# Optimization experiments

Measured on AMD Instinct MI355X. Metric: run time of the kernel, lower is better.

The kernel has to match this reference:

```python
import jax, jax.numpy as jnp
import numpy as np

K = 1.0          # manifold curvature parameter (Lorentz hyperboloid <x,x>_L = -K)
NUM_HEADS = 16
LN_EPS = 1e-5
MID_EPS = 1e-8


def add_time(space):
    # lift a space-like vector onto the hyperboloid: x0 = sqrt(||s||^2 + K)
    t = jnp.sqrt(jnp.sum(space * space, axis=-1, keepdims=True) + K)
    return jnp.concatenate([t, space], axis=-1)


def hlinear(x, W, b):
    # Lorentz linear: dense map on full ambient vector -> space part, recompute time
    return add_time(jnp.einsum('...d,od->...o', x, W) + b)


def hyp_layernorm(x, g, b):
    s = x[..., 1:]
    mu = jnp.mean(s, axis=-1, keepdims=True)
    var = jnp.mean((s - mu) ** 2, axis=-1, keepdims=True)
    s = (s - mu) * jax.lax.rsqrt(var + LN_EPS) * g + b
    return add_time(s)


def hyp_relu(x):
    return add_time(jax.nn.relu(x[..., 1:]))


def lorentz_norm(v):
    # sqrt(|<v,v>_L|) with clamp for numerical safety
    inner = -v[..., 0] ** 2 + jnp.sum(v[..., 1:] ** 2, axis=-1)
    return jnp.sqrt(jnp.maximum(jnp.abs(inner), MID_EPS))


def midpoint_pair(z, x):
    # manifold.midpoint(stack([z, x], dim=-2)).squeeze(): mean then project back
    ave = 0.5 * (z + x)
    return jnp.sqrt(K) * ave / lorentz_norm(ave)[..., None]


def attention(x, Wq, bq, Wk, bk, Wv, bv, Wo, bo):
    B, S, D = x.shape
    dim = D - 1
    H = NUM_HEADS
    dh = dim // H

    def split_heads(t):
        # drop time, split space into heads, re-lift each head onto hyperboloid
        s = t[..., 1:].reshape(B, S, H, dh).transpose(0, 2, 1, 3)  # [B,H,S,dh]
        return add_time(s)                                          # [B,H,S,dh+1]

    qh = split_heads(hlinear(x, Wq, bq))
    kh = split_heads(hlinear(x, Wk, bk))
    vh = split_heads(hlinear(x, Wv, bv))

    # pairwise Lorentz inner product; scores = -d_L^2 / sqrt(dh)
    inner = (jnp.einsum('bhid,bhjd->bhij', qh[..., 1:], kh[..., 1:])
             - qh[..., 0][..., :, None] * kh[..., 0][..., None, :])
    scores = (2.0 / K + 2.0 * inner) / jnp.sqrt(jnp.asarray(dh, x.dtype))
    att = jax.nn.softmax(scores, axis=-1)

    # Lorentz midpoint aggregation of values (weights sum to 1)
    ave = jnp.einsum('bhij,bhjd->bhid', att, vh)
    out = jnp.sqrt(K) * ave / lorentz_norm(ave)[..., None]  # [B,H,S,dh+1]

    # concat head space parts, re-lift, output projection
    out_space = out[..., 1:].transpose(0, 2, 1, 3).reshape(B, S, dim)
    return hlinear(add_time(out_space), Wo, bo)


def reference(x, Wq, bq, Wk, bk, Wv, bv, Wo, bo, ln1_g, ln1_b, W1, c1, W2, c2, ln2_g, ln2_b):
    z = attention(x, Wq, bq, Wk, bk, Wv, bv, Wo, bo)
    x = midpoint_pair(z, x)
    x = hyp_layernorm(x, ln1_g, ln1_b)
    h = hyp_relu(hlinear(x, W1, c1))
    z = hlinear(h, W2, c2)
    x = midpoint_pair(z, x)
    x = hyp_layernorm(x, ln2_g, ln2_b)
    return x


def setup_inputs() -> dict:
    key = jax.random.key(0)
    ks = jax.random.split(key, 12)
    B, S, dim, mlp = 4, 1024, 1024, 4096
    D = dim + 1
    sc = 0.02
    x = add_time(jax.random.normal(ks[0], (B, S, dim), dtype=jnp.float32))
    return {
        'x': x,
        'Wq': sc * jax.random.normal(ks[1], (dim, D), dtype=jnp.float32),
        'bq': jnp.zeros((dim,), jnp.float32),
        'Wk': sc * jax.random.normal(ks[2], (dim, D), dtype=jnp.float32),
        'bk': jnp.zeros((dim,), jnp.float32),
        'Wv': sc * jax.random.normal(ks[3], (dim, D), dtype=jnp.float32),
        'bv': jnp.zeros((dim,), jnp.float32),
        'Wo': sc * jax.random.normal(ks[4], (dim, D), dtype=jnp.float32),
        'bo': jnp.zeros((dim,), jnp.float32),
        'ln1_g': jnp.ones((dim,), jnp.float32),
        'ln1_b': jnp.zeros((dim,), jnp.float32),
        'W1': sc * jax.random.normal(ks[5], (mlp, D), dtype=jnp.float32),
        'c1': jnp.zeros((mlp,), jnp.float32),
        'W2': sc * jax.random.normal(ks[6], (dim, mlp + 1), dtype=jnp.float32),
        'c2': jnp.zeros((dim,), jnp.float32),
        'ln2_g': jnp.ones((dim,), jnp.float32),
        'ln2_b': jnp.zeros((dim,), jnp.float32),
    }
```

## Files before the change

### kernel.cpp

```cpp
#include <hip/hip_runtime.h>

typedef unsigned short u16;
typedef unsigned int   u32;
typedef short bf16x8 __attribute__((ext_vector_type(8)));
typedef float f32x4  __attribute__((ext_vector_type(4)));

#define NTOK 4096
#define SEQ  1024

__device__ __forceinline__ u16 f2bf(float f){
  union { float f; u32 u; } x; x.f = f;
  u32 r = (x.u + 0x7FFFu + ((x.u >> 16) & 1u)) >> 16;
  return (u16)r;
}
__device__ __forceinline__ float bf2f(u16 u){
  union { u32 u; float f; } x; x.u = ((u32)u) << 16; return x.f;
}
__device__ __forceinline__ void gl_lds16(const void* gp, void* lp){
  __builtin_amdgcn_global_load_lds(
      (const __attribute__((address_space(1))) u32*)gp,
      (__attribute__((address_space(3))) u32*)lp, 16, 0, 0);
}

__global__ __launch_bounds__(256) void conv_x(const float* __restrict__ x,
                                              u16* __restrict__ xs, float* __restrict__ xt){
  int t = blockIdx.x * 256 + threadIdx.x;
  int tok = t >> 10, i = t & 1023;
  xs[t] = f2bf(x[(size_t)tok * 1025 + 1 + i]);
  if (i == 0) xt[tok] = x[(size_t)tok * 1025];
}

__global__ __launch_bounds__(256) void conv_w_all(
    const float* __restrict__ Wq, const float* __restrict__ Wk,
    const float* __restrict__ Wv, const float* __restrict__ Wo,
    const float* __restrict__ W1, const float* __restrict__ W2,
    u16* __restrict__ wqkv, u16* __restrict__ wo_s, u16* __restrict__ w1_s, u16* __restrict__ w2_s,
    float* __restrict__ wqkv0, float* __restrict__ wo0, float* __restrict__ w10, float* __restrict__ w20)
{
  int t = blockIdx.x * 256 + threadIdx.x;
  const int M1 = 1 << 20;
  const float* W; u16* Wb; float* w0; int shift; int idx;
  if (t < 4 * M1){
    int region = t >> 20; idx = t & (M1 - 1); shift = 10;
    if (region == 0)      { W = Wq; Wb = wqkv;          w0 = wqkv0; }
    else if (region == 1) { W = Wk; Wb = wqkv + M1;     w0 = wqkv0 + 1024; }
    else if (region == 2) { W = Wv; Wb = wqkv + 2 * M1; w0 = wqkv0 + 2048; }
    else                  { W = Wo; Wb = wo_s;          w0 = wo0; }
  } else if (t < 8 * M1){
    idx = t - 4 * M1; shift = 10; W = W1; Wb = w1_s; w0 = w10;
  } else {
    idx = t - 8 * M1; shift = 12; W = W2; Wb = w2_s; w0 = w20;
  }
  int Kin = 1 << shift;
  int r = idx >> shift, i = idx & (Kin - 1);
  Wb[idx] = f2bf(W[(size_t)r * (Kin + 1) + 1 + i]);
  if (i == 0) w0[r] = W[(size_t)r * (Kin + 1)];
}

__global__ __launch_bounds__(256) void v_transpose(const u16* __restrict__ qkv,
                                                   const float* __restrict__ vtm,
                                                   u16* __restrict__ vT){
  __shared__ u16 tile[64 * 72];
  const int tid = threadIdx.x;
  const int kt = blockIdx.x, bh = blockIdx.y;
  const int b = bh >> 4, h = bh & 15;
  #pragma unroll
  for (int i = 0; i < 2; i++){
    int c = tid * 2 + i;
    int key = c >> 3, fc = c & 7;
    uint4 v = *(const uint4*)(qkv + ((size_t)(b * 1024 + kt * 64 + key)) * 3072 + 2048 + h * 64 + fc * 8);
    *(uint4*)&tile[key * 72 + fc * 8] = v;
  }
  __syncthreads();
  for (int c = tid; c < 520; c += 256){
    int vtr = c >> 3, kc = c & 7;
    union { uint4 v; u16 s[8]; } d;
    if (vtr == 0){
      #pragma unroll
      for (int j = 0; j < 8; j++) d.s[j] = f2bf(vtm[(size_t)bh * 1024 + kt * 64 + kc * 8 + j]);
    } else {
      int f = vtr - 1;
      #pragma unroll
      for (int j = 0; j < 8; j++) d.s[j] = tile[(kc * 8 + j) * 72 + f];
    }
    *(uint4*)(vT + ((size_t)bh * 65 + vtr) * 1024 + kt * 64 + kc * 8) = d.v;
  }
}

__global__ __launch_bounds__(256) void gemm_bt(
    const u16* __restrict__ A, int lda, const u16* __restrict__ Bm, int ldb,
    const float* __restrict__ at, int at_mode, const float* __restrict__ b0,
    const float* __restrict__ bias_a, const float* __restrict__ bias_b, const float* __restrict__ bias_c,
    u16* __restrict__ Cbf, int ldc, int Kslice, int mode,
    float* __restrict__ qtv, float* __restrict__ ktv, float* __restrict__ vtm,
    float* __restrict__ rowsq)
{
  __shared__ u16 As[2][128 * 64];
  __shared__ u16 Bs[2][128 * 64];
  const int tid = threadIdx.x;
  const int w = tid >> 6, l = tid & 63;
  const int l15 = l & 15, q = l >> 4;
  const int m0 = blockIdx.y * 128, n0 = blockIdx.x * 128;
  const int ks = blockIdx.z;
  const int kbeg = ks * Kslice;
  const int kend = kbeg + Kslice;
  const int wr = w >> 1, wc = w & 1;
  f32x4 acc[4][4] = {};

  auto stage = [&](int kt, int buf){
    #pragma unroll
    for (int half = 0; half < 2; half++){
      #pragma unroll
      for (int i = 0; i < 2; i++){
        int s = (w * 2 + i) * 64 + l;
        int row = s >> 2;
        int kc = ((s & 3) - (s >> 3)) & 3;
        gl_lds16(A  + (size_t)(m0 + row) * lda + kt + half * 32 + kc * 8,
                 &As[buf][half * 4096 + (w * 2 + i) * 512]);
        gl_lds16(Bm + (size_t)(n0 + row) * ldb + kt + half * 32 + kc * 8,
                 &Bs[buf][half * 4096 + (w * 2 + i) * 512]);
      }
    }
  };
  auto compute = [&](int buf, int half){
    bf16x8 af[4], bfr[4];
    #pragma unroll
    for (int i = 0; i < 4; i++){
      int row = wr * 64 + i * 16 + l15;
      int slot = row * 4 + ((q + (row >> 1)) & 3);
      af[i] = *(const bf16x8*)&As[buf][half * 4096 + slot * 8];
    }
    #pragma unroll
    for (int j = 0; j < 4; j++){
      int row = wc * 64 + j * 16 + l15;
      int slot = row * 4 + ((q + (row >> 1)) & 3);
      bfr[j] = *(const bf16x8*)&Bs[buf][half * 4096 + slot * 8];
    }
    #pragma unroll
    for (int i = 0; i < 4; i++)
      #pragma unroll
      for (int j = 0; j < 4; j++)
        acc[i][j] = __builtin_amdgcn_mfma_f32_16x16x32_bf16(af[i], bfr[j], acc[i][j], 0, 0, 0);
  };

  stage(kbeg, 0);
  for (int kt = kbeg; kt < kend; kt += 128){
    __syncthreads();
    if (kt + 64 < kend) stage(kt + 64, 1);
    compute(0, 0); compute(0, 1);
    __syncthreads();
    if (kt + 128 < kend) stage(kt + 128, 0);
    compute(1, 0); compute(1, 1);
  }

  const size_t slice_off = (size_t)ks * (size_t)(gridDim.y * 128) * ldc;
  #pragma unroll
  for (int i = 0; i < 4; i++){
    float atv[4];
    #pragma unroll
    for (int r = 0; r < 4; r++){
      float a = at[m0 + wr * 64 + i * 16 + q * 4 + r];
      atv[r] = at_mode ? sqrtf(a + 1.f) : a;
    }
    float p[4] = {0.f, 0.f, 0.f, 0.f};
    #pragma unroll
    for (int j = 0; j < 4; j++){
      int col = n0 + wc * 64 + j * 16 + l15;
      float b0v = b0[col];
      float bv;
      if (mode == 0) bv = (col < 1024) ? bias_a[col] : (col < 2048) ? bias_b[col - 1024] : bias_c[col - 2048];
      else bv = bias_a[col];
      #pragma unroll
      for (int r = 0; r < 4; r++){
        size_t row = (size_t)(m0 + wr * 64 + i * 16 + q * 4 + r);
        float add = (ks == 0) ? (atv[r] * b0v + bv) : 0.f;
        float v = acc[i][j][r] + add;
        if (mode == 2) v = fmaxf(v, 0.f);
        Cbf[slice_off + row * ldc + col] = f2bf(v);
        if (mode != 1) p[r] += v * v;
      }
    }
    if (mode != 1){
      #pragma unroll
      for (int r = 0; r < 4; r++){
        float s = p[r];
        s += __shfl_xor(s, 1, 64); s += __shfl_xor(s, 2, 64);
        s += __shfl_xor(s, 4, 64); s += __shfl_xor(s, 8, 64);
        if (l15 == 0){
          int row = m0 + wr * 64 + i * 16 + q * 4 + r;
          if (mode == 2){
            atomicAdd(&rowsq[row], s);
          } else {
            int ch = (n0 + wc * 64) >> 6;
            int bb = row >> 10, sidx = row & 1023;
            float t = sqrtf(s + 1.f);
            if (ch < 16)      qtv[((size_t)bb * 16 + ch) * 1024 + sidx] = t;
            else if (ch < 32) ktv[((size_t)bb * 16 + ch - 16) * 1024 + sidx] = t;
            else              vtm[((size_t)bb * 16 + ch - 32) * 1024 + sidx] = t;
          }
        }
      }
    }
  }
}

__global__ __launch_bounds__(512) void attn_kernel(
    const u16* __restrict__ qkv, const float* __restrict__ qt,
    const float* __restrict__ ktm, const u16* __restrict__ vT,
    u16* __restrict__ aout, float* __restrict__ aot_sq)
{
  __shared__ u16 smem[30720];
  u16* Qlds = smem;
  u16* Kl0 = smem + 8192;
  u16* Kl1 = smem + 12288;
  u16* Vl0 = smem + 16384;
  u16* Vl1 = smem;
  u16* Plds = smem + 21504;
  const int tid = threadIdx.x;
  const int w = tid >> 6, l = tid & 63;
  const int l15 = l & 15, qd = l >> 4;
  const int q0 = blockIdx.x * 128;
  const int bh = blockIdx.y;
  const int b = bh >> 4, h = bh & 15;
  const size_t tokbase = (size_t)b << 10;

  #pragma unroll
  for (int i = 0; i < 2; i++){
    int c = i * 512 + w * 64 + l;
    int row = c >> 3, kc = ((c & 7) - row) & 7;
    gl_lds16(qkv + (tokbase + q0 + row) * 3072 + h * 64 + kc * 8, &Qlds[(i * 512 + w * 64) * 8]);
  }
  __syncthreads();
  bf16x8 aq[2];
  {
    int row = w * 16 + l15;
    #pragma unroll
    for (int kk = 0; kk < 2; kk++)
      aq[kk] = *(const bf16x8*)&Qlds[(row * 8 + ((kk * 4 + qd + row) & 7)) * 8];
  }
  float tq[4];
  #pragma unroll
  for (int r = 0; r < 4; r++)
    tq[r] = qt[(size_t)bh * SEQ + q0 + w * 16 + qd * 4 + r];

  auto stage_kv = [&](int kt, int buf){
    u16* K = buf ? Kl1 : Kl0;
    u16* V = buf ? Vl1 : Vl0;
    int c = w * 64 + l;
    int row = c >> 3, kc = ((c & 7) - row) & 7;
    gl_lds16(qkv + (tokbase + kt * 64 + row) * 3072 + 1024 + h * 64 + kc * 8, &K[w * 512]);
    gl_lds16(vT + ((size_t)bh * 65 + row) * 1024 + kt * 64 + kc * 8, &V[w * 512]);
    if (w == 0 && l < 8)
      gl_lds16(vT + ((size_t)bh * 65 + 64) * 1024 + kt * 64 + (l & 7) * 8, &V[4096]);
  };

  float mrow[4] = {-1e30f, -1e30f, -1e30f, -1e30f};
  f32x4 acco[5] = {};

  stage_kv(0, 0);
  for (int kt = 0; kt < 16; kt++){
    __syncthreads();
    if (kt + 1 < 16) stage_kv(kt + 1, (kt + 1) & 1);
    u16* K = (kt & 1) ? Kl1 : Kl0;
    u16* V = (kt & 1) ? Vl1 : Vl0;

    float sc[4][4];
    float mx[4] = {-1e30f, -1e30f, -1e30f, -1e30f};
    #pragma unroll
    for (int ct = 0; ct < 4; ct++){
      f32x4 z = {0.f, 0.f, 0.f, 0.f};
      int key = ct * 16 + l15;
      #pragma unroll
      for (int kk = 0; kk < 2; kk++){
        bf16x8 bk = *(const bf16x8*)&K[(key * 8 + ((kk * 4 + qd + key) & 7)) * 8];
        z = __builtin_amdgcn_mfma_f32_16x16x32_bf16(aq[kk], bk, z, 0, 0, 0);
      }
      float tk = ktm[(size_t)bh * SEQ + kt * 64 + key];
      #pragma unroll
      for (int r = 0; r < 4; r++){
        float s = 0.25f + 0.25f * (z[r] - tq[r] * tk);
        sc[ct][r] = s;
        mx[r] = fmaxf(mx[r], s);
      }
    }
    #pragma unroll
    for (int r = 0; r < 4; r++){
      #pragma unroll
      for (int msk = 1; msk < 16; msk <<= 1)
        mx[r] = fmaxf(mx[r], __shfl_xor(mx[r], msk, 64));
      float mnew = fmaxf(mrow[r], mx[r]);
      float alpha = __expf(mrow[r] - mnew);
      mrow[r] = mnew;
      #pragma unroll
      for (int co = 0; co < 5; co++) acco[co][r] *= alpha;
      mx[r] = mnew;
    }
    #pragma unroll
    for (int ct = 0; ct < 4; ct++)
      #pragma unroll
      for (int r = 0; r < 4; r++)
        Plds[w * 1152 + (qd * 4 + r) * 72 + ct * 16 + l15] = f2bf(__expf(sc[ct][r] - mx[r]));
    asm volatile("s_waitcnt lgkmcnt(0)" ::: "memory");
    bf16x8 ap[2];
    #pragma unroll
    for (int kk = 0; kk < 2; kk++)
      ap[kk] = *(const bf16x8*)&Plds[w * 1152 + l15 * 72 + kk * 32 + qd * 8];
    #pragma unroll
    for (int co = 0; co < 5; co++){
      int vtr = co * 16 + l15;
      #pragma unroll
      for (int kk = 0; kk < 2; kk++){
        bf16x8 bv = *(const bf16x8*)&V[(vtr * 8 + ((kk * 4 + qd + vtr) & 7)) * 8];
        acco[co] = __builtin_amdgcn_mfma_f32_16x16x32_bf16(ap[kk], bv, acco[co], 0, 0, 0);
      }
    }
  }
  #pragma unroll
  for (int r = 0; r < 4; r++){
    float ss = 0.f;
    #pragma unroll
    for (int co = 0; co < 5; co++){
      int col = co * 16 + l15;
      float v = acco[co][r];
      if (col == 0) ss -= v * v;
      else if (col < 65) ss += v * v;
    }
    #pragma unroll
    for (int msk = 1; msk < 16; msk <<= 1) ss += __shfl_xor(ss, msk, 64);
    float v0b = __shfl(acco[0][r], l & 48, 64);
    float sp = ss + v0b * v0b;
    float rn = rsqrtf(fmaxf(fabsf(ss), 1e-8f));
    size_t rowg = tokbase + q0 + w * 16 + qd * 4 + r;
    if (l15 == 0) atomicAdd(&aot_sq[rowg], sp * rn * rn);
    #pragma unroll
    for (int co = 0; co < 5; co++){
      int col = co * 16 + l15;
      if (col >= 1 && col < 65)
        aout[rowg * 1024 + h * 64 + col - 1] = f2bf(acco[co][r] * rn);
    }
  }
}

__device__ __forceinline__ float block_sum(float v, float* red){
  int tid = threadIdx.x;
  #pragma unroll
  for (int m = 1; m < 64; m <<= 1) v += __shfl_xor(v, m, 64);
  __syncthreads();
  if ((tid & 63) == 0) red[tid >> 6] = v;
  __syncthreads();
  return red[0] + red[1] + red[2] + red[3];
}

__global__ __launch_bounds__(256) void mid_ln(
    const u16* __restrict__ z, const u16* __restrict__ xsb, const float* __restrict__ xtv,
    const float* __restrict__ gam, const float* __restrict__ bet,
    u16* __restrict__ ob, float* __restrict__ ot,
    float* __restrict__ ofull, int mode_out, int nsl)
{
  __shared__ float red[4];
  const int tid = threadIdx.x;
  const int tok = blockIdx.x;
  float zv[4], xv[4], xtime;
  xtime = xtv[tok];
  {
    const u16* xr = xsb + (size_t)tok * 1024;
    #pragma unroll
    for (int j = 0; j < 4; j++) xv[j] = bf2f(xr[tid + j * 256]);
  }
  {
    #pragma unroll
    for (int j = 0; j < 4; j++) zv[j] = 0.f;
    for (int s = 0; s < nsl; s++){
      const u16* zs = z + (size_t)s * NTOK * 1024 + (size_t)tok * 1024;
      #pragma unroll
      for (int j = 0; j < 4; j++) zv[j] += bf2f(zs[tid + j * 256]);
    }
  }
  float ssz = 0.f;
  #pragma unroll
  for (int j = 0; j < 4; j++) ssz += zv[j] * zv[j];
  ssz = block_sum(ssz, red);
  float tz = sqrtf(ssz + 1.f);
  float av[4]; float ssa = 0.f;
  #pragma unroll
  for (int j = 0; j < 4; j++){ av[j] = 0.5f * (zv[j] + xv[j]); ssa += av[j] * av[j]; }
  ssa = block_sum(ssa, red);
  float avt = 0.5f * (tz + xtime);
  float rn = rsqrtf(fmaxf(fabsf(ssa - avt * avt), 1e-8f));
  float uv[4]; float su = 0.f, squ = 0.f;
  #pragma unroll
  for (int j = 0; j < 4; j++){ uv[j] = av[j] * rn; su += uv[j]; squ += uv[j] * uv[j]; }
  su = block_sum(su, red);
  squ = block_sum(squ, red);
  float mu = su * (1.f / 1024.f);
  float var = squ * (1.f / 1024.f) - mu * mu;
  float rv = rsqrtf(fmaxf(var, 0.f) + 1e-5f);
  float sv[4]; float sss = 0.f;
  #pragma unroll
  for (int j = 0; j < 4; j++){
    int i = tid + j * 256;
    sv[j] = (uv[j] - mu) * rv * gam[i] + bet[i];
    sss += sv[j] * sv[j];
  }
  sss = block_sum(sss, red);
  float tout = sqrtf(sss + 1.f);
  if (mode_out == 0){
    #pragma unroll
    for (int j = 0; j < 4; j++){
      int i = tid + j * 256;
      ob[(size_t)tok * 1024 + i] = f2bf(sv[j]);
    }
    if (tid == 0) ot[tok] = tout;
  } else {
    float* orow = ofull + (size_t)tok * 1025;
    #pragma unroll
    for (int j = 0; j < 4; j++) orow[1 + tid + j * 256] = sv[j];
    if (tid == 0) orow[0] = tout;
  }
}

extern "C" void kernel_launch(void* const* d_in, const int* in_sizes, int n_in,
                              void* d_out, int out_size, void* d_ws, size_t ws_size,
                              hipStream_t stream){
  const float* x   = (const float*)d_in[0];
  const float* Wq  = (const float*)d_in[1];
  const float* bq  = (const float*)d_in[2];
  const float* Wk  = (const float*)d_in[3];
  const float* bk  = (const float*)d_in[4];
  const float* Wv  = (const float*)d_in[5];
  const float* bv  = (const float*)d_in[6];
  const float* Wo  = (const float*)d_in[7];
  const float* bo  = (const float*)d_in[8];
  const float* g1  = (const float*)d_in[9];
  const float* be1 = (const float*)d_in[10];
  const float* W1  = (const float*)d_in[11];
  const float* c1  = (const float*)d_in[12];
  const float* W2  = (const float*)d_in[13];
  const float* c2  = (const float*)d_in[14];
  const float* g2  = (const float*)d_in[15];
  const float* be2 = (const float*)d_in[16];
  float* out = (float*)d_out;

  char* p = (char*)d_ws;
  auto take = [&](size_t n){ char* r = p; p += (n + 255) & ~(size_t)255; return r; };
  u16*   xs    = (u16*)  take((size_t)NTOK * 1024 * 2);
  float* xt    = (float*)take(NTOK * 4);
  u16*   wqkv  = (u16*)  take((size_t)3072 * 1024 * 2);
  float* wqkv0 = (float*)take(3072 * 4);
  u16*   wo_s  = (u16*)  take((size_t)1024 * 1024 * 2);
  float* wo0   = (float*)take(1024 * 4);
  u16*   w1_s  = (u16*)  take((size_t)4096 * 1024 * 2);
  float* w10   = (float*)take(4096 * 4);
  u16*   w2_s  = (u16*)  take((size_t)1024 * 4096 * 2);
  float* w20   = (float*)take(1024 * 4);
  u16*   qkvb  = (u16*)  take((size_t)NTOK * 3072 * 2);
  float* qtv   = (float*)take((size_t)64 * 1024 * 4);
  float* ktv   = (float*)take((size_t)64 * 1024 * 4);
  float* vtm   = (float*)take((size_t)64 * 1024 * 4);
  u16*   vT    = (u16*)  take((size_t)64 * 65 * 1024 * 2);
  u16*   aoutb = (u16*)  take((size_t)NTOK * 1024 * 2);
  float* sqbuf = (float*)take((size_t)2 * NTOK * 4);
  float* aot_sq = sqbuf;
  float* htv_sq = sqbuf + NTOK;
  u16*   zbuf  = (u16*)  take((size_t)4 * NTOK * 1024 * 2);
  u16*   x1b   = (u16*)  take((size_t)NTOK * 1024 * 2);
  float* x1t   = (float*)take(NTOK * 4);
  u16*   hbuf  = (u16*)  take((size_t)NTOK * 4096 * 2);

  hipMemsetAsync(sqbuf, 0, (size_t)2 * NTOK * 4, stream);

  conv_x<<<NTOK * 1024 / 256, 256, 0, stream>>>(x, xs, xt);
  conv_w_all<<<(12 * 1024 * 1024) / 256, 256, 0, stream>>>(
      Wq, Wk, Wv, Wo, W1, W2, wqkv, wo_s, w1_s, w2_s, wqkv0, wo0, w10, w20);

  gemm_bt<<<dim3(24, 32), 256, 0, stream>>>(xs, 1024, wqkv, 1024, xt, 0, wqkv0,
      bq, bk, bv, qkvb, 3072, 1024, 0, qtv, ktv, vtm, nullptr);
  v_transpose<<<dim3(16, 64), 256, 0, stream>>>(qkvb, vtm, vT);
  attn_kernel<<<dim3(8, 64), 512, 0, stream>>>(qkvb, qtv, ktv, vT, aoutb, aot_sq);
  gemm_bt<<<dim3(8, 32, 2), 256, 0, stream>>>(aoutb, 1024, wo_s, 1024, aot_sq, 1, wo0,
      bo, nullptr, nullptr, zbuf, 1024, 512, 1, nullptr, nullptr, nullptr, nullptr);
  mid_ln<<<NTOK, 256, 0, stream>>>(zbuf, xs, xt, g1, be1,
      x1b, x1t, nullptr, 0, 2);
  gemm_bt<<<dim3(32, 32), 256, 0, stream>>>(x1b, 1024, w1_s, 1024, x1t, 0, w10,
      c1, nullptr, nullptr, hbuf, 4096, 1024, 2, nullptr, nullptr, nullptr, htv_sq);
  gemm_bt<<<dim3(8, 32, 4), 256, 0, stream>>>(hbuf, 4096, w2_s, 4096, htv_sq, 1, w20,
      c2, nullptr, nullptr, zbuf, 1024, 1024, 1, nullptr, nullptr, nullptr, nullptr);
  mid_ln<<<NTOK, 256, 0, stream>>>(zbuf, x1b, x1t, g2, be2,
      nullptr, nullptr, out, 1, 4);
}
```

Measured before the change: 429.7 us.

## Rewrite GEMM as 256x256 tile, 8-wave, finely interleaved load/MFMA pipeline

The bf16 GEMM moves from 128x128 tiles with 4 waves to 256x256 tiles with 8 waves. A hand-scheduled loop splits each K-step into quadrants, interleaving LDS fragment loads, async global-to-LDS staging, explicit vmcnt waits and barriers, and raises priority around the MFMA bursts. It also adds an XCD-aware workgroup swizzle and changes the split-K factor for the output projection, with the first mid_ln reduce count updated to match. The goal is more data reuse per tile and better overlap of memory with compute. The trade-offs are a larger register footprint (8x4 accumulators) and fewer workgroups, which could leave some CUs idle on the smaller GEMMs.

```diff
diff --git a/kernel.cpp b/kernel.cpp
--- a/kernel.cpp
+++ b/kernel.cpp
@@ -7,6 +7,9 @@
 
 #define NTOK 4096
 #define SEQ  1024
+
+#define BARRIER() __builtin_amdgcn_s_barrier()
+#define VMCNT(n) asm volatile("s_waitcnt vmcnt(" #n ")" ::: "memory")
 
 __device__ __forceinline__ u16 f2bf(float f){
   union { float f; u32 u; } x; x.f = f;
@@ -87,94 +90,153 @@
   }
 }
 
-__global__ __launch_bounds__(256) void gemm_bt(
-    const u16* __restrict__ A, int lda, const u16* __restrict__ Bm, int ldb,
+__global__ __launch_bounds__(512, 2) void gemm_bt(
+    const u16* __restrict__ Ag, int lda, const u16* __restrict__ Bg, int ldb,
     const float* __restrict__ at, int at_mode, const float* __restrict__ b0,
     const float* __restrict__ bias_a, const float* __restrict__ bias_b, const float* __restrict__ bias_c,
     u16* __restrict__ Cbf, int ldc, int Kslice, int mode,
     float* __restrict__ qtv, float* __restrict__ ktv, float* __restrict__ vtm,
     float* __restrict__ rowsq)
 {
-  __shared__ u16 As[2][128 * 64];
-  __shared__ u16 Bs[2][128 * 64];
+  __shared__ u16 smem[65536];
   const int tid = threadIdx.x;
   const int w = tid >> 6, l = tid & 63;
   const int l15 = l & 15, q = l >> 4;
-  const int m0 = blockIdx.y * 128, n0 = blockIdx.x * 128;
+  const int wr = w >> 2, wc = w & 3;
+  const int gx = gridDim.x;
+  const int nwg = gx * gridDim.y;
+  const int lin = blockIdx.y * gx + blockIdx.x;
+  const int swz = (lin & 7) * (nwg >> 3) + (lin >> 3);
+  const int m0 = (swz / gx) * 256, n0 = (swz % gx) * 256;
   const int ks = blockIdx.z;
   const int kbeg = ks * Kslice;
-  const int kend = kbeg + Kslice;
-  const int wr = w >> 1, wc = w & 1;
-  f32x4 acc[4][4] = {};
-
-  auto stage = [&](int kt, int buf){
-    #pragma unroll
-    for (int half = 0; half < 2; half++){
-      #pragma unroll
-      for (int i = 0; i < 2; i++){
-        int s = (w * 2 + i) * 64 + l;
-        int row = s >> 2;
-        int kc = ((s & 3) - (s >> 3)) & 3;
-        gl_lds16(A  + (size_t)(m0 + row) * lda + kt + half * 32 + kc * 8,
-                 &As[buf][half * 4096 + (w * 2 + i) * 512]);
-        gl_lds16(Bm + (size_t)(n0 + row) * ldb + kt + half * 32 + kc * 8,
-                 &Bs[buf][half * 4096 + (w * 2 + i) * 512]);
-      }
+
+  f32x4 acc[8][4] = {};
+  bf16x8 af[4][2], b0f[2][2], b1f[2][2];
+
+  auto stageA = [&](int kt, int buf, int qm){
+    #pragma unroll
+    for (int ii = 0; ii < 2; ii++){
+      int s = (w * 2 + ii) * 64 + l;
+      int kk = s >> 9, rem = s & 511;
+      int ridx = rem >> 2, cp = rem & 3;
+      int kc = (cp - (ridx >> 1)) & 3;
+      int trow = ((ridx >> 6) << 7) + qm * 64 + (ridx & 63);
+      gl_lds16(Ag + (size_t)(m0 + trow) * lda + kt + kk * 32 + kc * 8,
+               &smem[(buf * 2 + qm) * 8192 + (w * 2 + ii) * 512]);
     }
   };
-  auto compute = [&](int buf, int half){
-    bf16x8 af[4], bfr[4];
-    #pragma unroll
-    for (int i = 0; i < 4; i++){
-      int row = wr * 64 + i * 16 + l15;
-      int slot = row * 4 + ((q + (row >> 1)) & 3);
-      af[i] = *(const bf16x8*)&As[buf][half * 4096 + slot * 8];
-    }
-    #pragma unroll
-    for (int j = 0; j < 4; j++){
-      int row = wc * 64 + j * 16 + l15;
-      int slot = row * 4 + ((q + (row >> 1)) & 3);
-      bfr[j] = *(const bf16x8*)&Bs[buf][half * 4096 + slot * 8];
-    }
-    #pragma unroll
-    for (int i = 0; i < 4; i++)
-      #pragma unroll
-      for (int j = 0; j < 4; j++)
-        acc[i][j] = __builtin_amdgcn_mfma_f32_16x16x32_bf16(af[i], bfr[j], acc[i][j], 0, 0, 0);
+  auto stageB = [&](int kt, int buf, int qn){
+    #pragma unroll
+    for (int ii = 0; ii < 2; ii++){
+      int s = (w * 2 + ii) * 64 + l;
+      int kk = s >> 9, rem = s & 511;
+      int ridx = rem >> 2, cp = rem & 3;
+      int kc = (cp - (ridx >> 1)) & 3;
+      int trow = ((ridx >> 5) << 6) + qn * 32 + (ridx & 31);
+      gl_lds16(Bg + (size_t)(n0 + trow) * ldb + kt + kk * 32 + kc * 8,
+               &smem[32768 + (buf * 2 + qn) * 8192 + (w * 2 + ii) * 512]);
+    }
   };
-
-  stage(kbeg, 0);
-  for (int kt = kbeg; kt < kend; kt += 128){
-    __syncthreads();
-    if (kt + 64 < kend) stage(kt + 64, 1);
-    compute(0, 0); compute(0, 1);
-    __syncthreads();
-    if (kt + 128 < kend) stage(kt + 128, 0);
-    compute(1, 0); compute(1, 1);
-  }
-
-  const size_t slice_off = (size_t)ks * (size_t)(gridDim.y * 128) * ldc;
-  #pragma unroll
-  for (int i = 0; i < 4; i++){
+  auto loadA = [&](int buf, int qm){
+    #pragma unroll
+    for (int i2 = 0; i2 < 4; i2++){
+      int ridx = wr * 64 + i2 * 16 + l15;
+      int slot = ridx * 4 + ((q + (ridx >> 1)) & 3);
+      #pragma unroll
+      for (int kk = 0; kk < 2; kk++)
+        af[i2][kk] = *(const bf16x8*)&smem[(buf * 2 + qm) * 8192 + kk * 4096 + slot * 8];
+    }
+  };
+  auto loadB = [&](int buf, int qn, bf16x8 (&bb)[2][2]){
+    #pragma unroll
+    for (int j2 = 0; j2 < 2; j2++){
+      int ridx = wc * 32 + j2 * 16 + l15;
+      int slot = ridx * 4 + ((q + (ridx >> 1)) & 3);
+      #pragma unroll
+      for (int kk = 0; kk < 2; kk++)
+        bb[j2][kk] = *(const bf16x8*)&smem[32768 + (buf * 2 + qn) * 8192 + kk * 4096 + slot * 8];
+    }
+  };
+  auto mma4 = [&](int qm, int qn, bf16x8 (&bb)[2][2]){
+    __builtin_amdgcn_s_setprio(1);
+    #pragma unroll
+    for (int i2 = 0; i2 < 4; i2++)
+      #pragma unroll
+      for (int j2 = 0; j2 < 2; j2++)
+        #pragma unroll
+        for (int kk = 0; kk < 2; kk++)
+          acc[qm * 4 + i2][qn * 2 + j2] = __builtin_amdgcn_mfma_f32_16x16x32_bf16(
+              af[i2][kk], bb[j2][kk], acc[qm * 4 + i2][qn * 2 + j2], 0, 0, 0);
+    __builtin_amdgcn_s_setprio(0);
+  };
+
+  stageA(kbeg, 0, 0);
+  stageB(kbeg, 0, 0);
+  stageB(kbeg, 0, 1);
+  stageA(kbeg, 0, 1);
+  stageA(kbeg + 64, 1, 0);
+  stageB(kbeg + 64, 1, 1);
+  stageA(kbeg + 64, 1, 1);
+  VMCNT(6);
+  BARRIER();
+
+  const int NI = Kslice >> 7;
+  for (int it = 0; it < NI; it++){
+    const int kb = kbeg + it * 128;
+    const bool more = (it + 1 < NI);
+    loadA(0, 0); loadB(0, 0, b0f);
+    stageB(kb + 64, 1, 0);
+    BARRIER(); mma4(0, 0, b0f); BARRIER();
+    loadB(0, 1, b1f);
+    if (more) stageA(kb + 128, 0, 0);
+    BARRIER(); mma4(0, 1, b1f); BARRIER();
+    loadA(0, 1);
+    if (more) stageB(kb + 128, 0, 1);
+    BARRIER(); mma4(1, 1, b1f); BARRIER();
+    loadB(0, 0, b0f);
+    if (more) stageA(kb + 128, 0, 1);
+    if (more) { VMCNT(6); } else { VMCNT(0); }
+    BARRIER(); mma4(1, 0, b0f); BARRIER();
+    loadA(1, 0); loadB(1, 0, b0f);
+    if (more) stageB(kb + 128, 0, 0);
+    BARRIER(); mma4(0, 0, b0f); BARRIER();
+    loadB(1, 1, b1f);
+    if (more) stageA(kb + 192, 1, 0);
+    BARRIER(); mma4(0, 1, b1f); BARRIER();
+    loadA(1, 1);
+    if (more) stageB(kb + 192, 1, 1);
+    BARRIER(); mma4(1, 1, b1f); BARRIER();
+    loadB(1, 0, b0f);
+    if (more) stageA(kb + 192, 1, 1);
+    if (more) { VMCNT(6); }
+    BARRIER(); mma4(1, 0, b0f); BARRIER();
+  }
+
+  const size_t Mtot = (size_t)gridDim.y * 256;
+  const size_t slice_off = (size_t)ks * Mtot * ldc;
+  #pragma unroll
+  for (int ai = 0; ai < 8; ai++){
+    const int rb = wr * 128 + (ai >> 2) * 64 + (ai & 3) * 16 + q * 4;
     float atv[4];
     #pragma unroll
     for (int r = 0; r < 4; r++){
-      float a = at[m0 + wr * 64 + i * 16 + q * 4 + r];
+      float a = at[m0 + rb + r];
       atv[r] = at_mode ? sqrtf(a + 1.f) : a;
     }
     float p[4] = {0.f, 0.f, 0.f, 0.f};
     #pragma unroll
-    for (int j = 0; j < 4; j++){
-      int col = n0 + wc * 64 + j * 16 + l15;
+    for (int bj = 0; bj < 4; bj++){
+      const int col = n0 + wc * 64 + (bj >> 1) * 32 + (bj & 1) * 16 + l15;
       float b0v = b0[col];
       float bv;
       if (mode == 0) bv = (col < 1024) ? bias_a[col] : (col < 2048) ? bias_b[col - 1024] : bias_c[col - 2048];
       else bv = bias_a[col];
       #pragma unroll
       for (int r = 0; r < 4; r++){
-        size_t row = (size_t)(m0 + wr * 64 + i * 16 + q * 4 + r);
+        size_t row = (size_t)(m0 + rb + r);
         float add = (ks == 0) ? (atv[r] * b0v + bv) : 0.f;
-        float v = acc[i][j][r] + add;
+        float v = acc[ai][bj][r] + add;
         if (mode == 2) v = fmaxf(v, 0.f);
         Cbf[slice_off + row * ldc + col] = f2bf(v);
         if (mode != 1) p[r] += v * v;
@@ -187,7 +249,7 @@
         s += __shfl_xor(s, 1, 64); s += __shfl_xor(s, 2, 64);
         s += __shfl_xor(s, 4, 64); s += __shfl_xor(s, 8, 64);
         if (l15 == 0){
-          int row = m0 + wr * 64 + i * 16 + q * 4 + r;
+          int row = m0 + rb + r;
           if (mode == 2){
             atomicAdd(&rowsq[row], s);
           } else {
@@ -473,17 +535,17 @@
   conv_w_all<<<(12 * 1024 * 1024) / 256, 256, 0, stream>>>(
       Wq, Wk, Wv, Wo, W1, W2, wqkv, wo_s, w1_s, w2_s, wqkv0, wo0, w10, w20);
 
-  gemm_bt<<<dim3(24, 32), 256, 0, stream>>>(xs, 1024, wqkv, 1024, xt, 0, wqkv0,
+  gemm_bt<<<dim3(12, 16), 512, 0, stream>>>(xs, 1024, wqkv, 1024, xt, 0, wqkv0,
       bq, bk, bv, qkvb, 3072, 1024, 0, qtv, ktv, vtm, nullptr);
-  v_transpose<<<dim3(16, 64), 256, 0, stream>>>(qkvb, vtm, vT);
+  v_transpose<<<dim3(16, 64), 512 / 2, 0, stream>>>(qkvb, vtm, vT);
   attn_kernel<<<dim3(8, 64), 512, 0, stream>>>(qkvb, qtv, ktv, vT, aoutb, aot_sq);
-  gemm_bt<<<dim3(8, 32, 2), 256, 0, stream>>>(aoutb, 1024, wo_s, 1024, aot_sq, 1, wo0,
-      bo, nullptr, nullptr, zbuf, 1024, 512, 1, nullptr, nullptr, nullptr, nullptr);
+  gemm_bt<<<dim3(4, 16, 4), 512, 0, stream>>>(aoutb, 1024, wo_s, 1024, aot_sq, 1, wo0,
+      bo, nullptr, nullptr, zbuf, 1024, 256, 1, nullptr, nullptr, nullptr, nullptr);
   mid_ln<<<NTOK, 256, 0, stream>>>(zbuf, xs, xt, g1, be1,
-      x1b, x1t, nullptr, 0, 2);
-  gemm_bt<<<dim3(32, 32), 256, 0, stream>>>(x1b, 1024, w1_s, 1024, x1t, 0, w10,
+      x1b, x1t, nullptr, 0, 4);
+  gemm_bt<<<dim3(16, 16), 512, 0, stream>>>(x1b, 1024, w1_s, 1024, x1t, 0, w10,
       c1, nullptr, nullptr, hbuf, 4096, 1024, 2, nullptr, nullptr, nullptr, htv_sq);
-  gemm_bt<<<dim3(8, 32, 4), 256, 0, stream>>>(hbuf, 4096, w2_s, 4096, htv_sq, 1, w20,
+  gemm_bt<<<dim3(4, 16, 4), 512, 0, stream>>>(hbuf, 4096, w2_s, 4096, htv_sq, 1, w20,
       c2, nullptr, nullptr, zbuf, 1024, 1024, 1, nullptr, nullptr, nullptr, nullptr);
   mid_ln<<<NTOK, 256, 0, stream>>>(zbuf, x1b, x1t, g2, be2,
       nullptr, nullptr, out, 1, 4);
```

Result: faster. 413.7 us (-3.7%).
